# Kernel tuning notes

Hardware: AMD Instinct MI355X
Metric: run time of the kernel (lower is better)

Reference implementation:

```python
import jax, jax.numpy as jnp
import numpy as np

COMMITMENT_COST = 0.25
N_EMBED = 1024
EMB_DIM = 256

def setup_inputs() -> dict:
    key = jax.random.key(0)
    k1, k2 = jax.random.split(key)
    z = jax.random.normal(k1, (32, EMB_DIM, 32, 32), dtype=jnp.float32)
    # embedding.weight.data.uniform_(-1/n_embed, 1/n_embed)
    embedding = jax.random.uniform(k2, (N_EMBED, EMB_DIM), dtype=jnp.float32,
                                   minval=-1.0 / N_EMBED, maxval=1.0 / N_EMBED)
    return {"z": z, "embedding": embedding}

def reference(z, embedding):
    # NCHW -> NHWC
    zp = jnp.transpose(z, (0, 2, 3, 1))            # [B,H,W,D]
    in_shape = zp.shape
    flat = zp.reshape(-1, in_shape[-1])            # [N,D]
    # squared L2 distances (argmin equivalent to p=2 cdist argmin)
    d2 = (jnp.sum(flat * flat, axis=1, keepdims=True)
          - 2.0 * (flat @ embedding.T)
          + jnp.sum(embedding * embedding, axis=1))  # [N,K]
    idx = jnp.argmin(d2, axis=1)                   # [N]
    # one-hot @ codebook == direct gather
    z_quant = embedding[idx].reshape(in_shape)     # [B,H,W,D]
    codebook_loss = jnp.mean((z_quant - jax.lax.stop_gradient(zp)) ** 2)
    commitment_loss = jnp.mean((zp - jax.lax.stop_gradient(z_quant)) ** 2)
    loss = codebook_loss + COMMITMENT_COST * commitment_loss
    # straight-through estimator
    z_st = zp + jax.lax.stop_gradient(z_quant - zp)
    z_st = jnp.transpose(z_st, (0, 3, 1, 2))       # NHWC -> NCHW
    return (z_st, loss, codebook_loss, commitment_loss)
```

## Files before the change

### kernel.cpp

```cpp
#include <hip/hip_runtime.h>
#include <hip/hip_bf16.h>
#include <stdint.h>


typedef short v8s __attribute__((ext_vector_type(8)));
typedef float v4f __attribute__((ext_vector_type(4)));

__device__ inline unsigned short f2bf(float f) {
    uint32_t u = __float_as_uint(f);
    return (unsigned short)((u + 0x7fffu + ((u >> 16) & 1u)) >> 16);
}

__global__ __launch_bounds__(256) void k_prep_e(const float* __restrict__ E,
                                                v8s* __restrict__ Esw,
                                                float* __restrict__ nE,
                                                float* __restrict__ accum,
                                                unsigned* __restrict__ done) {
    __shared__ float Ef[16][264];
    int q = blockIdx.x, tid = threadIdx.x;
    const float4* Ein = (const float4*)(E + ((size_t)q << 12));
#pragma unroll
    for (int i = 0; i < 4; i++) {
        int f4 = i * 256 + tid;
        int row = f4 >> 6, c4 = (f4 & 63) << 2;
        *(float4*)&Ef[row][c4] = Ein[f4];
    }
    __syncthreads();
    {
        int c = tid >> 4, l = tid & 15;
        float s = 0.f;
#pragma unroll
        for (int j = 0; j < 16; j++) { float v = Ef[c][l + 16 * j]; s += v * v; }
#pragma unroll
        for (int off = 1; off < 16; off <<= 1) s += __shfl_xor(s, off);
        if (l == 0) nE[q * 16 + c] = 0.5f * s;
    }
#pragma unroll
    for (int i = 0; i < 2; i++) {
        int u = tid + i * 256;
        int um = u & 15, ug = (u >> 4) & 3, udc = (u >> 6) & 7;
        int d0 = udc * 32 + ug * 8;
        union { v8s v; unsigned short s[8]; } pk;
#pragma unroll
        for (int e = 0; e < 8; e++) pk.s[e] = f2bf(Ef[um][d0 + e]);
        Esw[((size_t)q << 9) + u] = pk.v;
    }
    if (q == 0 && tid == 0) { accum[0] = 0.f; done[0] = 0u; }
}

__global__ __launch_bounds__(512) void k_main(
        const v8s* __restrict__ Esw,
        const float* __restrict__ nE,
        const float* __restrict__ z,
        const float* __restrict__ E,
        float* __restrict__ out,
        float* __restrict__ accum,
        unsigned* __restrict__ done) {
    __shared__ v8s B[2][4096];
    __shared__ float nEl[1024];
    __shared__ float nrmLds[128];
    __shared__ __align__(16) int idxLds[128];
    __shared__ float w8[8];

    int tid = threadIdx.x;
    int lane = tid & 63, w = tid >> 6;
    int g = lane >> 4, m = lane & 15;
    int R0 = blockIdx.x << 7;
    int b = R0 >> 10, hw0 = R0 & 1023;

#define STAGE(ch, buf)                                                        \
    {                                                                         \
        _Pragma("unroll")                                                     \
        for (int j = 0; j < 8; j++) {                                         \
            __builtin_amdgcn_global_load_lds(                                 \
                (const __attribute__((address_space(1))) void*)               \
                    (Esw + ((size_t)(ch) << 12) + (j << 9) + (w << 6) + lane),\
                (__attribute__((address_space(3))) void*)                     \
                    &B[buf][(j << 9) + (w << 6)],                             \
                16, 0, 0);                                                    \
        }                                                                     \
    }

    STAGE(0, 0);

    {
        int q = tid & 31, dblk = tid >> 5;
        const float* zp = z + ((size_t)b << 18) + hw0 + (q << 2);
#pragma unroll
        for (int s = 0; s < 2; s++) {
            float4 L[8];
#pragma unroll
            for (int j = 0; j < 8; j++)
                L[j] = *(const float4*)(zp + (size_t)(((dblk << 4) + (s << 3) + j) << 10));
            const float* Lf = (const float*)L;
            int slot = (dblk << 1) + s;
#pragma unroll
            for (int c = 0; c < 4; c++) {
                union { v8s v; unsigned short u[8]; } pk;
#pragma unroll
                for (int j = 0; j < 8; j++) pk.u[j] = f2bf(Lf[j * 4 + c]);
                int row = (q << 2) + c;
                int sw = slot ^ ((row ^ (row >> 2)) & 7);
                *(v8s*)((char*)&B[1][0] + (row << 9) + (sw << 4)) = pk.v;
            }
        }
    }
#pragma unroll
    for (int i = 0; i < 2; i++) nEl[tid + i * 512] = nE[tid + i * 512];
    __syncthreads();

    v8s a[8];
    {
        int row = (w << 4) + m;
        int f = (row ^ (row >> 2)) & 7;
#pragma unroll
        for (int dc = 0; dc < 8; dc++) {
            int sw = ((dc << 2) + g) ^ f;
            a[dc] = *(const v8s*)((const char*)&B[1][0] + (row << 9) + (sw << 4));
        }
        float nrm = 0.f;
#pragma unroll
        for (int dc = 0; dc < 8; dc++) {
            union { v8s v; unsigned short u[8]; } un; un.v = a[dc];
#pragma unroll
            for (int j = 0; j < 8; j++) {
                float v = __uint_as_float((uint32_t)un.u[j] << 16);
                nrm = fmaf(v, v, nrm);
            }
        }
        nrm += __shfl_xor(nrm, 16);
        nrm += __shfl_xor(nrm, 32);
        if (g == 0) nrmLds[row] = nrm;
    }
    __syncthreads();
    float best[4]; int bidx[4];
#pragma unroll
    for (int r = 0; r < 4; r++) { best[r] = 3.4e38f; bidx[r] = 0; }

#pragma unroll 2
    for (int ct = 0; ct < 8; ct++) {
        int cur = ct & 1;
        if (ct < 7) STAGE(ct + 1, cur ^ 1);
        float ne[8];
#pragma unroll
        for (int t = 0; t < 8; t++) ne[t] = nEl[(ct << 7) + (t << 4) + m];
        v4f acc[8];
#pragma unroll
        for (int t = 0; t < 8; t++) acc[t] = (v4f){0.f, 0.f, 0.f, 0.f};
#pragma unroll
        for (int dc = 0; dc < 8; dc++) {
#pragma unroll
            for (int t = 0; t < 8; t++) {
                v8s bf = B[cur][t * 512 + dc * 64 + g * 16 + m];
                acc[t] = __builtin_amdgcn_mfma_f32_16x16x32_bf16(a[dc], bf, acc[t], 0, 0, 0);
            }
        }
#pragma unroll
        for (int t = 0; t < 8; t++) {
            int code = (ct << 7) + (t << 4) + m;
#pragma unroll
            for (int r = 0; r < 4; r++) {
                float s0 = ne[t] - acc[t][r];
                if (s0 < best[r]) { best[r] = s0; bidx[r] = code; }
            }
        }
        __syncthreads();
    }

    float lsum = 0.f;
#pragma unroll
    for (int r = 0; r < 4; r++) {
        uint32_t sb = __float_as_uint(best[r]);
        sb = (sb & 0x80000000u) ? ~sb : (sb | 0x80000000u);
        unsigned long long pk = ((unsigned long long)sb << 32) | (uint32_t)bidx[r];
#pragma unroll
        for (int off = 1; off < 16; off <<= 1) {
            unsigned long long o = __shfl_xor(pk, off);
            if (o < pk) pk = o;
        }
        int row = (w << 4) + (g << 2) + r;
        if (m == 0) {
            idxLds[row] = (int)(pk & 0xffffffffu);
            uint32_t t = (uint32_t)(pk >> 32);
            float sw = __uint_as_float((t & 0x80000000u) ? (t & 0x7fffffffu) : ~t);
            lsum += 2.0f * sw + nrmLds[row];
        }
    }
#pragma unroll
    for (int off = 1; off < 64; off <<= 1) lsum += __shfl_xor(lsum, off);
    if (lane == 0) w8[w] = lsum;
    __syncthreads();

    {
        int q = tid & 31, dd = tid >> 5;
        int4 kk = *(const int4*)&idxLds[q << 2];
        float* ob = out + ((size_t)b << 18) + hw0 + (q << 2);
#pragma unroll
        for (int i = 0; i < 4; i++) {
            int d0 = (dd + (i << 4)) << 2;
            float4 e0 = *(const float4*)(E + ((size_t)kk.x << 8) + d0);
            float4 e1 = *(const float4*)(E + ((size_t)kk.y << 8) + d0);
            float4 e2 = *(const float4*)(E + ((size_t)kk.z << 8) + d0);
            float4 e3 = *(const float4*)(E + ((size_t)kk.w << 8) + d0);
            const float* p0 = &e0.x; const float* p1 = &e1.x;
            const float* p2 = &e2.x; const float* p3 = &e3.x;
#pragma unroll
            for (int r = 0; r < 4; r++) {
                float4 v; v.x = p0[r]; v.y = p1[r]; v.z = p2[r]; v.w = p3[r];
                *(float4*)(ob + ((size_t)(d0 + r) << 10)) = v;
            }
        }
    }

    if (tid == 0) {
        float s8 = 0.f;
#pragma unroll
        for (int i = 0; i < 8; i++) s8 += w8[i];
        atomicAdd(accum, s8);
        __threadfence();
        unsigned old = atomicAdd(done, 1u);
        if (old == 255u) {
            float s = atomicAdd(accum, 0.f) * (1.0f / 8388608.0f);
            out[8388608] = 1.25f * s;
            out[8388609] = s;
            out[8388610] = s;
        }
    }
#undef STAGE
}

extern "C" void kernel_launch(void* const* d_in, const int* in_sizes, int n_in,
                              void* d_out, int out_size, void* d_ws, size_t ws_size,
                              hipStream_t stream) {
    const float* z = (const float*)d_in[0];
    const float* E = (const float*)d_in[1];
    char* ws = (char*)d_ws;
    v8s*      Esw   = (v8s*)(ws);
    float*    nE    = (float*)(ws + 524288);
    float*    accum = (float*)(ws + 528384);
    unsigned* done  = (unsigned*)(ws + 528388);
    float* out = (float*)d_out;

    hipLaunchKernelGGL(k_prep_e, dim3(64),  dim3(256), 0, stream, E, Esw, nE, accum, done);
    hipLaunchKernelGGL(k_main,   dim3(256), dim3(512), 0, stream,
                       Esw, nE, z, E, out, accum, done);
}
```

Before: 120.7 us.

## Split codebook across two blocks per row tile and move gather to epilogue kernel

The main kernel now launches two blocks per 128-row tile, each scanning half the codebook with half the LDS. Partial argmins are merged through a 64-bit atomicMin on a packed score/index array, which the prep kernel initialises. A new epilogue kernel performs the codebook gather, the transposed output write and the loss reduction. The aim is to double the block count and raise occupancy on the large GPU. The cost is an extra kernel launch, global atomics and a round trip through global memory for indices and norms.

```diff
diff --git a/kernel.cpp b/kernel.cpp
--- a/kernel.cpp
+++ b/kernel.cpp
@@ -14,6 +14,7 @@
 __global__ __launch_bounds__(256) void k_prep_e(const float* __restrict__ E,
                                                 v8s* __restrict__ Esw,
                                                 float* __restrict__ nE,
+                                                unsigned long long* __restrict__ idxPk,
                                                 float* __restrict__ accum,
                                                 unsigned* __restrict__ done) {
     __shared__ float Ef[16][264];
@@ -25,6 +26,11 @@
         int row = f4 >> 6, c4 = (f4 & 63) << 2;
         *(float4*)&Ef[row][c4] = Ein[f4];
     }
+    {
+        int u = (q << 8) + tid;
+        idxPk[(size_t)(u << 1)]     = ~0ull;
+        idxPk[(size_t)(u << 1) + 1] = ~0ull;
+    }
     __syncthreads();
     {
         int c = tid >> 4, l = tid & 15;
@@ -48,126 +54,123 @@
     if (q == 0 && tid == 0) { accum[0] = 0.f; done[0] = 0u; }
 }
 
-__global__ __launch_bounds__(512) void k_main(
+__global__ __launch_bounds__(512, 4) void k_main(
         const v8s* __restrict__ Esw,
         const float* __restrict__ nE,
         const float* __restrict__ z,
-        const float* __restrict__ E,
-        float* __restrict__ out,
-        float* __restrict__ accum,
-        unsigned* __restrict__ done) {
-    __shared__ v8s B[2][4096];
-    __shared__ float nEl[1024];
-    __shared__ float nrmLds[128];
-    __shared__ __align__(16) int idxLds[128];
-    __shared__ float w8[8];
+        unsigned long long* __restrict__ idxPk,
+        float* __restrict__ nrmG) {
+    __shared__ v8s B[2][2048];
+    __shared__ float nEl[512];
 
     int tid = threadIdx.x;
     int lane = tid & 63, w = tid >> 6;
     int g = lane >> 4, m = lane & 15;
-    int R0 = blockIdx.x << 7;
+    int r_tile = blockIdx.x >> 1, h = blockIdx.x & 1;
+    int R0 = r_tile << 7;
     int b = R0 >> 10, hw0 = R0 & 1023;
+
+    {
+        int q = tid & 31, dblk = tid >> 5;
+        const float* zp = z + ((size_t)b << 18) + hw0 + (q << 2);
+#pragma unroll
+        for (int s = 0; s < 2; s++) {
+            float4 L[8];
+#pragma unroll
+            for (int j = 0; j < 8; j++)
+                L[j] = *(const float4*)(zp + (size_t)(((dblk << 4) + (s << 3) + j) << 10));
+            const float* Lf = (const float*)L;
+            int slot = (dblk << 1) + s;
+#pragma unroll
+            for (int c = 0; c < 4; c++) {
+                union { v8s v; unsigned short u[8]; } pk;
+#pragma unroll
+                for (int j = 0; j < 8; j++) pk.u[j] = f2bf(Lf[j * 4 + c]);
+                int row = (q << 2) + c;
+                int sw = slot ^ ((row ^ (row >> 2)) & 7);
+                *(v8s*)((char*)&B[0][0] + (row << 9) + (sw << 4)) = pk.v;
+            }
+        }
+    }
+    nEl[tid & 511] = nE[(h << 9) + (tid & 511)];
+    __syncthreads();
+
+    v8s a[8];
+    {
+        int row = (w << 4) + m;
+        int f = (row ^ (row >> 2)) & 7;
+#pragma unroll
+        for (int dc = 0; dc < 8; dc++) {
+            int sw = ((dc << 2) + g) ^ f;
+            a[dc] = *(const v8s*)((const char*)&B[0][0] + (row << 9) + (sw << 4));
+        }
+        if (h == 0) {
+            float nrm = 0.f;
+#pragma unroll
+            for (int dc = 0; dc < 8; dc++) {
+                union { v8s v; unsigned short u[8]; } un; un.v = a[dc];
+#pragma unroll
+                for (int j = 0; j < 8; j++) {
+                    float v = __uint_as_float((uint32_t)un.u[j] << 16);
+                    nrm = fmaf(v, v, nrm);
+                }
+            }
+            nrm += __shfl_xor(nrm, 16);
+            nrm += __shfl_xor(nrm, 32);
+            if (g == 0) nrmG[R0 + row] = nrm;
+        }
+    }
+    __syncthreads();
 
 #define STAGE(ch, buf)                                                        \
     {                                                                         \
         _Pragma("unroll")                                                     \
-        for (int j = 0; j < 8; j++) {                                         \
+        for (int j = 0; j < 4; j++) {                                         \
             __builtin_amdgcn_global_load_lds(                                 \
                 (const __attribute__((address_space(1))) void*)               \
-                    (Esw + ((size_t)(ch) << 12) + (j << 9) + (w << 6) + lane),\
+                    (Esw + ((size_t)(h) << 14) + ((size_t)(ch) << 11)         \
+                         + (j << 9) + (w << 6) + lane),                       \
                 (__attribute__((address_space(3))) void*)                     \
                     &B[buf][(j << 9) + (w << 6)],                             \
                 16, 0, 0);                                                    \
         }                                                                     \
     }
 
+    float best[4]; int bidx[4];
+#pragma unroll
+    for (int r = 0; r < 4; r++) { best[r] = 3.4e38f; bidx[r] = 0; }
+
     STAGE(0, 0);
-
-    {
-        int q = tid & 31, dblk = tid >> 5;
-        const float* zp = z + ((size_t)b << 18) + hw0 + (q << 2);
-#pragma unroll
-        for (int s = 0; s < 2; s++) {
-            float4 L[8];
-#pragma unroll
-            for (int j = 0; j < 8; j++)
-                L[j] = *(const float4*)(zp + (size_t)(((dblk << 4) + (s << 3) + j) << 10));
-            const float* Lf = (const float*)L;
-            int slot = (dblk << 1) + s;
-#pragma unroll
-            for (int c = 0; c < 4; c++) {
-                union { v8s v; unsigned short u[8]; } pk;
-#pragma unroll
-                for (int j = 0; j < 8; j++) pk.u[j] = f2bf(Lf[j * 4 + c]);
-                int row = (q << 2) + c;
-                int sw = slot ^ ((row ^ (row >> 2)) & 7);
-                *(v8s*)((char*)&B[1][0] + (row << 9) + (sw << 4)) = pk.v;
-            }
-        }
-    }
-#pragma unroll
-    for (int i = 0; i < 2; i++) nEl[tid + i * 512] = nE[tid + i * 512];
-    __syncthreads();
-
-    v8s a[8];
-    {
-        int row = (w << 4) + m;
-        int f = (row ^ (row >> 2)) & 7;
-#pragma unroll
-        for (int dc = 0; dc < 8; dc++) {
-            int sw = ((dc << 2) + g) ^ f;
-            a[dc] = *(const v8s*)((const char*)&B[1][0] + (row << 9) + (sw << 4));
-        }
-        float nrm = 0.f;
-#pragma unroll
-        for (int dc = 0; dc < 8; dc++) {
-            union { v8s v; unsigned short u[8]; } un; un.v = a[dc];
-#pragma unroll
-            for (int j = 0; j < 8; j++) {
-                float v = __uint_as_float((uint32_t)un.u[j] << 16);
-                nrm = fmaf(v, v, nrm);
-            }
-        }
-        nrm += __shfl_xor(nrm, 16);
-        nrm += __shfl_xor(nrm, 32);
-        if (g == 0) nrmLds[row] = nrm;
-    }
-    __syncthreads();
-    float best[4]; int bidx[4];
-#pragma unroll
-    for (int r = 0; r < 4; r++) { best[r] = 3.4e38f; bidx[r] = 0; }
-
 #pragma unroll 2
     for (int ct = 0; ct < 8; ct++) {
         int cur = ct & 1;
+        __syncthreads();
         if (ct < 7) STAGE(ct + 1, cur ^ 1);
-        float ne[8];
-#pragma unroll
-        for (int t = 0; t < 8; t++) ne[t] = nEl[(ct << 7) + (t << 4) + m];
-        v4f acc[8];
-#pragma unroll
-        for (int t = 0; t < 8; t++) acc[t] = (v4f){0.f, 0.f, 0.f, 0.f};
+        float ne[4];
+#pragma unroll
+        for (int t = 0; t < 4; t++) ne[t] = nEl[(ct << 6) + (t << 4) + m];
+        v4f acc[4];
+#pragma unroll
+        for (int t = 0; t < 4; t++) acc[t] = (v4f){0.f, 0.f, 0.f, 0.f};
 #pragma unroll
         for (int dc = 0; dc < 8; dc++) {
 #pragma unroll
-            for (int t = 0; t < 8; t++) {
+            for (int t = 0; t < 4; t++) {
                 v8s bf = B[cur][t * 512 + dc * 64 + g * 16 + m];
                 acc[t] = __builtin_amdgcn_mfma_f32_16x16x32_bf16(a[dc], bf, acc[t], 0, 0, 0);
             }
         }
 #pragma unroll
-        for (int t = 0; t < 8; t++) {
-            int code = (ct << 7) + (t << 4) + m;
+        for (int t = 0; t < 4; t++) {
+            int code = (h << 9) + (ct << 6) + (t << 4) + m;
 #pragma unroll
             for (int r = 0; r < 4; r++) {
                 float s0 = ne[t] - acc[t][r];
                 if (s0 < best[r]) { best[r] = s0; bidx[r] = code; }
             }
         }
-        __syncthreads();
-    }
-
-    float lsum = 0.f;
+    }
+
 #pragma unroll
     for (int r = 0; r < 4; r++) {
         uint32_t sb = __float_as_uint(best[r]);
@@ -178,55 +181,62 @@
             unsigned long long o = __shfl_xor(pk, off);
             if (o < pk) pk = o;
         }
-        int row = (w << 4) + (g << 2) + r;
         if (m == 0) {
-            idxLds[row] = (int)(pk & 0xffffffffu);
-            uint32_t t = (uint32_t)(pk >> 32);
-            float sw = __uint_as_float((t & 0x80000000u) ? (t & 0x7fffffffu) : ~t);
-            lsum += 2.0f * sw + nrmLds[row];
-        }
-    }
-#pragma unroll
-    for (int off = 1; off < 64; off <<= 1) lsum += __shfl_xor(lsum, off);
-    if (lane == 0) w8[w] = lsum;
-    __syncthreads();
-
-    {
-        int q = tid & 31, dd = tid >> 5;
-        int4 kk = *(const int4*)&idxLds[q << 2];
-        float* ob = out + ((size_t)b << 18) + hw0 + (q << 2);
+            int row = (w << 4) + (g << 2) + r;
+            atomicMin(&idxPk[R0 + row], pk);
+        }
+    }
+#undef STAGE
+}
+
+__global__ __launch_bounds__(256) void k_epi(const unsigned long long* __restrict__ idxPk,
+                                             const float* __restrict__ nrmG,
+                                             const float* __restrict__ E,
+                                             float* __restrict__ accum,
+                                             unsigned* __restrict__ done,
+                                             float* __restrict__ out) {
+    int j = blockIdx.x, t = threadIdx.x;
+    int b = j >> 6, d0 = (j & 63) << 2;
+    const unsigned long long* pkRow = idxPk + (b << 10) + (t << 2);
+    unsigned long long p0 = pkRow[0], p1 = pkRow[1], p2 = pkRow[2], p3 = pkRow[3];
+    float4 e0 = *(const float4*)(E + ((size_t)(uint32_t)p0 << 8) + d0);
+    float4 e1 = *(const float4*)(E + ((size_t)(uint32_t)p1 << 8) + d0);
+    float4 e2 = *(const float4*)(E + ((size_t)(uint32_t)p2 << 8) + d0);
+    float4 e3 = *(const float4*)(E + ((size_t)(uint32_t)p3 << 8) + d0);
+    const float* q0 = &e0.x; const float* q1 = &e1.x;
+    const float* q2 = &e2.x; const float* q3 = &e3.x;
+    float* ob = out + ((size_t)b << 18) + ((size_t)d0 << 10) + (t << 2);
+#pragma unroll
+    for (int i = 0; i < 4; i++) {
+        float4 v; v.x = q0[i]; v.y = q1[i]; v.z = q2[i]; v.w = q3[i];
+        *(float4*)(ob + (size_t)i * 1024) = v;
+    }
+    if ((j & 63) == 0) {
+        float ls = 0.f;
+        const unsigned long long* pp[4] = {&p0, &p1, &p2, &p3};
 #pragma unroll
         for (int i = 0; i < 4; i++) {
-            int d0 = (dd + (i << 4)) << 2;
-            float4 e0 = *(const float4*)(E + ((size_t)kk.x << 8) + d0);
-            float4 e1 = *(const float4*)(E + ((size_t)kk.y << 8) + d0);
-            float4 e2 = *(const float4*)(E + ((size_t)kk.z << 8) + d0);
-            float4 e3 = *(const float4*)(E + ((size_t)kk.w << 8) + d0);
-            const float* p0 = &e0.x; const float* p1 = &e1.x;
-            const float* p2 = &e2.x; const float* p3 = &e3.x;
-#pragma unroll
-            for (int r = 0; r < 4; r++) {
-                float4 v; v.x = p0[r]; v.y = p1[r]; v.z = p2[r]; v.w = p3[r];
-                *(float4*)(ob + ((size_t)(d0 + r) << 10)) = v;
-            }
-        }
-    }
-
-    if (tid == 0) {
-        float s8 = 0.f;
-#pragma unroll
-        for (int i = 0; i < 8; i++) s8 += w8[i];
-        atomicAdd(accum, s8);
+            uint32_t sc = (uint32_t)(*pp[i] >> 32);
+            float s = __uint_as_float((sc & 0x80000000u) ? (sc & 0x7fffffffu) : ~sc);
+            ls += 2.0f * s + nrmG[(b << 10) + (t << 2) + i];
+        }
+#pragma unroll
+        for (int off = 1; off < 64; off <<= 1) ls += __shfl_xor(ls, off);
+        __shared__ float w4[4];
+        if ((t & 63) == 0) w4[t >> 6] = ls;
+        __syncthreads();
+        if (t == 0) atomicAdd(accum, w4[0] + w4[1] + w4[2] + w4[3]);
+    }
+    if (t == 0) {
         __threadfence();
         unsigned old = atomicAdd(done, 1u);
-        if (old == 255u) {
+        if (old == 2047u) {
             float s = atomicAdd(accum, 0.f) * (1.0f / 8388608.0f);
             out[8388608] = 1.25f * s;
             out[8388609] = s;
             out[8388610] = s;
         }
     }
-#undef STAGE
 }
 
 extern "C" void kernel_launch(void* const* d_in, const int* in_sizes, int n_in,
@@ -235,13 +245,18 @@
     const float* z = (const float*)d_in[0];
     const float* E = (const float*)d_in[1];
     char* ws = (char*)d_ws;
-    v8s*      Esw   = (v8s*)(ws);
-    float*    nE    = (float*)(ws + 524288);
-    float*    accum = (float*)(ws + 528384);
-    unsigned* done  = (unsigned*)(ws + 528388);
+    v8s*                Esw   = (v8s*)(ws);
+    float*              nE    = (float*)(ws + 524288);
+    float*              accum = (float*)(ws + 528384);
+    unsigned*           done  = (unsigned*)(ws + 528388);
+    float*              nrmG  = (float*)(ws + 528392);
+    unsigned long long* idxPk = (unsigned long long*)(ws + 659464);
     float* out = (float*)d_out;
 
-    hipLaunchKernelGGL(k_prep_e, dim3(64),  dim3(256), 0, stream, E, Esw, nE, accum, done);
-    hipLaunchKernelGGL(k_main,   dim3(256), dim3(512), 0, stream,
-                       Esw, nE, z, E, out, accum, done);
-}
+    hipLaunchKernelGGL(k_prep_e, dim3(64),   dim3(256), 0, stream,
+                       E, Esw, nE, idxPk, accum, done);
+    hipLaunchKernelGGL(k_main,   dim3(512),  dim3(512), 0, stream,
+                       Esw, nE, z, idxPk, nrmG);
+    hipLaunchKernelGGL(k_epi,    dim3(2048), dim3(256), 0, stream,
+                       idxPk, nrmG, E, accum, done, out);
+}
```

After: 188.6 us. +56.2%, slower.
